# Performance work log

Measured on AMD Instinct MI355X. Metric: run time of the kernel, lower is better.

Reference implementation:

```python
import jax, jax.numpy as jnp
import numpy as np

H, W = 256, 256          # detector height/width (pixels)
DELX, DELY = 2.0, 2.0    # detector pixel pitch (mm)
EPS = 1e-8


def _rot(theta, phi, gamma):
    """R = Rz(theta) @ Ry(phi) @ Rx(gamma)."""
    ct, st = jnp.cos(theta), jnp.sin(theta)
    cp, sp = jnp.cos(phi), jnp.sin(phi)
    cg, sg = jnp.cos(gamma), jnp.sin(gamma)
    one = jnp.ones_like(ct); zero = jnp.zeros_like(ct)
    Rz = jnp.stack([jnp.stack([ct, -st, zero]), jnp.stack([st, ct, zero]), jnp.stack([zero, zero, one])])
    Ry = jnp.stack([jnp.stack([cp, zero, sp]), jnp.stack([zero, one, zero]), jnp.stack([-sp, zero, cp])])
    Rx = jnp.stack([jnp.stack([one, zero, zero]), jnp.stack([zero, cg, -sg]), jnp.stack([zero, sg, cg])])
    return Rz @ Ry @ Rx


def _make_xrays(sdr, rotations, translations):
    """Source point (3,) and detector-plane targets (H*W, 3)."""
    R = _rot(rotations[0], rotations[1], rotations[2])
    source = sdr * R[:, 0] + translations      # (3,)
    center = -sdr * R[:, 0] + translations     # detector center, opposite side
    u, v = R[:, 1], R[:, 2]                    # detector in-plane basis (unit)
    t = (jnp.arange(-(H // 2), H // 2, dtype=jnp.float32) + 1.0) * DELX  # (H,)
    s = (jnp.arange(-(W // 2), W // 2, dtype=jnp.float32) + 1.0) * DELY  # (W,)
    # cartesian_prod(t, s) @ [u; v]  ->  t_i * u + s_j * v   (t varies slowest)
    targets = t[:, None, None] * u + s[None, :, None] * v    # (H, W, 3)
    targets = targets.reshape(-1, 3) + center                # (H*W, 3)
    return source, targets


def _raytrace(volume, spacing, source, targets):
    """Siddon ray-tracing: line integral of volume along each source->target ray."""
    nx, ny, nz = volume.shape                       # planes per axis = n + 1
    dims = jnp.array([nx + 1, ny + 1, nz + 1], dtype=jnp.float32)
    sdd = targets - source + EPS                     # (R, 3) ray direction (unnormalized)

    # Entry/exit parametric range [alphamin, alphamax] per ray
    a0 = (0.0 * spacing - source) / sdd              # alpha at first planes
    a1 = ((dims - 1.0) * spacing - source) / sdd     # alpha at last planes
    amin = jnp.max(jnp.minimum(a0, a1), axis=-1, keepdims=True)  # (R, 1)
    amax = jnp.min(jnp.maximum(a0, a1), axis=-1, keepdims=True)  # (R, 1)

    # Alphas at every axis-aligned plane intersection
    ax = (jnp.arange(nx + 1, dtype=jnp.float32) * spacing[0] - source[0]) / sdd[:, 0:1]
    ay = (jnp.arange(ny + 1, dtype=jnp.float32) * spacing[1] - source[1]) / sdd[:, 1:2]
    az = (jnp.arange(nz + 1, dtype=jnp.float32) * spacing[2] - source[2]) / sdd[:, 2:3]
    alphas = jnp.concatenate([ax, ay, az], axis=-1)  # (R, P) with P = nx+ny+nz+3

    # Out-of-range alphas -> amax (amax is itself a kept plane intersection, so the
    # extra trailing segments have zero length; equivalent to the torch NaN trick
    # but NaN-free, so gradients stay clean).
    good = (alphas >= amin) & (alphas <= amax)
    alphas = jnp.where(good, alphas, amax)
    alphas = jnp.sort(alphas, axis=-1)

    amid = 0.5 * (alphas[:, :-1] + alphas[:, 1:])    # (R, P-1) segment midpoints
    step = jnp.diff(alphas, axis=-1)                 # (R, P-1) segment lengths (alpha units)

    # Voxel containing each midpoint (trunc == floor for in-volume points)
    pts = source + amid[..., None] * sdd[:, None, :] # (R, P-1, 3)
    idx = jnp.trunc(pts / spacing).astype(jnp.int32)
    idx = jnp.clip(idx, 0, jnp.array([nx - 1, ny - 1, nz - 1], dtype=jnp.int32))
    vox = volume[idx[..., 0], idx[..., 1], idx[..., 2]]  # (R, P-1)

    drr = jnp.sum(vox * step, axis=-1)               # (R,)
    raylength = jnp.linalg.norm(sdd, axis=-1)        # convert alpha units -> mm
    return drr * raylength


def setup_inputs() -> dict:
    key = jax.random.key(0)
    volume = jax.random.uniform(key, (256, 256, 256), dtype=jnp.float32)  # CT attenuation
    spacing = jnp.ones((3,), dtype=jnp.float32)
    sdr = jnp.asarray(300.0, dtype=jnp.float32)
    rotations = jnp.array([np.pi, 0.0, np.pi / 2], dtype=jnp.float32)     # theta, phi, gamma
    translations = jnp.array([128.0, 128.0, 128.0], dtype=jnp.float32)    # volume center
    return {"volume": volume, "spacing": spacing, "sdr": sdr,
            "rotations": rotations, "translations": translations}


def reference(volume, spacing, sdr, rotations, translations):
    source, targets = _make_xrays(sdr, rotations, translations)
    return _raytrace(volume, spacing, source, targets)  # (H*W,)
```

## Files before the change

kernel.cpp:

```cpp
#include <hip/hip_runtime.h>
#include <math.h>


#define NPLANE 256
constexpr int TPR = 16;

__device__ __forceinline__ float palpha(int i, float sp, float src, float rd) {
    return fmaf((float)i, sp, -src) * rd;
}

__global__ __launch_bounds__(256) void drr_kernel(
    const float* __restrict__ vol,
    const float* __restrict__ spacing,
    const float* __restrict__ sdrp,
    const float* __restrict__ rot,
    const float* __restrict__ trans,
    float* __restrict__ out)
{
    int gid  = blockIdx.x * blockDim.x + threadIdx.x;
    int part = gid & (TPR - 1);
    int rl   = gid / TPR;

    float theta = rot[0], phi = rot[1], gam = rot[2];
    float ct = cosf(theta), st = sinf(theta);
    float cp = cosf(phi),   sp_ = sinf(phi);
    float cg = cosf(gam),   sg = sinf(gam);

    float r0x = ct * cp, r0y = st * cp, r0z = -sp_;
    float ux = ct * sp_ * sg - st * cg, uy = st * sp_ * sg + ct * cg, uz = cp * sg;
    float vx = ct * sp_ * cg + st * sg, vy = st * sp_ * cg - ct * sg, vz = cp * cg;

    float cost_u = fabsf(ux) * 65536.f + fabsf(uy) * 256.f + fabsf(uz);
    float cost_v = fabsf(vx) * 65536.f + fabsf(vy) * 256.f + fabsf(vz);
    bool tfast = cost_u < cost_v;
    int ti = tfast ? (rl & 255) : (rl >> 8);
    int si = tfast ? (rl >> 8) : (rl & 255);

    float sdr = sdrp[0];
    float tx = trans[0], ty = trans[1], tz = trans[2];

    float sx = sdr * r0x + tx,  sy = sdr * r0y + ty,  sz = sdr * r0z + tz;
    float cxx = -sdr * r0x + tx, cxy = -sdr * r0y + ty, cxz = -sdr * r0z + tz;

    float tval = (float)(ti - 127) * 2.0f;
    float sval = (float)(si - 127) * 2.0f;

    float gx = tval * ux + sval * vx + cxx;
    float gy = tval * uy + sval * vy + cxy;
    float gz = tval * uz + sval * vz + cxz;

    float sdx = gx - sx + 1e-8f;
    float sdy = gy - sy + 1e-8f;
    float sdz = gz - sz + 1e-8f;

    float spx = spacing[0], spy = spacing[1], spz = spacing[2];

    float rdx = 1.0f / sdx, rdy = 1.0f / sdy, rdz = 1.0f / sdz;

    float a0x = palpha(0, spx, sx, rdx), a1x = palpha(NPLANE, spx, sx, rdx);
    float a0y = palpha(0, spy, sy, rdy), a1y = palpha(NPLANE, spy, sy, rdy);
    float a0z = palpha(0, spz, sz, rdz), a1z = palpha(NPLANE, spz, sz, rdz);

    float amin = fmaxf(fmaxf(fminf(a0x, a1x), fminf(a0y, a1y)), fminf(a0z, a1z));
    float amax = fminf(fminf(fmaxf(a0x, a1x), fmaxf(a0y, a1y)), fmaxf(a0z, a1z));

    float acc = 0.f;

    if (amax > amin) {
        float range = amax - amin;
        constexpr float inv = 1.0f / (float)TPR;
        float lo = fmaf(range, (float)part * inv, amin);
        float hi = (part == TPR - 1) ? INFINITY
                                     : fmaf(range, (float)(part + 1) * inv, amin);
        float end = fminf(hi, amax);

        int ix, iy, iz, dix, diy, diz;
        float nxx, nxy, nxz;

        #define SETUP(SP, SRC, SDD, RD, I, DI, NXT)                                \
        {                                                                          \
            float q = fmaf(lo, SDD, SRC) / (SP);                                   \
            q = fminf(fmaxf(q, -1.f), 257.f);                                      \
            if ((SDD) > 0.f) {                                                     \
                DI = 1;                                                            \
                I = (int)ceilf(q);                                                 \
                while (I > 0 && palpha(I - 1, SP, SRC, RD) >= lo) --I;             \
                while (I <= NPLANE && palpha(I, SP, SRC, RD) < lo) ++I;            \
                NXT = (I <= NPLANE) ? palpha(I, SP, SRC, RD) : INFINITY;           \
            } else {                                                               \
                DI = -1;                                                           \
                I = (int)floorf(q);                                                \
                while (I < NPLANE && palpha(I + 1, SP, SRC, RD) >= lo) ++I;        \
                while (I >= 0 && palpha(I, SP, SRC, RD) < lo) --I;                 \
                NXT = (I >= 0) ? palpha(I, SP, SRC, RD) : INFINITY;                \
            }                                                                      \
        }

        SETUP(spx, sx, sdx, rdx, ix, dix, nxx)
        SETUP(spy, sy, sdy, rdy, iy, diy, nxy)
        SETUP(spz, sz, sdz, rdz, iz, diz, nxz)
        #undef SETUP

        float ispx = 1.0f / spx, ispy = 1.0f / spy, ispz = 1.0f / spz;

        #define ADVANCE_MERGE()                                                    \
            if (nxx == cur) { ix += dix;                                           \
                nxx = ((unsigned)ix <= NPLANE) ? palpha(ix, spx, sx, rdx)          \
                                               : INFINITY; }                       \
            if (nxy == cur) { iy += diy;                                           \
                nxy = ((unsigned)iy <= NPLANE) ? palpha(iy, spy, sy, rdy)          \
                                               : INFINITY; }                       \
            if (nxz == cur) { iz += diz;                                           \
                nxz = ((unsigned)iz <= NPLANE) ? palpha(iz, spz, sz, rdz)          \
                                               : INFINITY; }

        #define SEG_ADDR(CUR, E, ADDR)                                             \
        {                                                                          \
            float amid = 0.5f * ((CUR) + (E));                                     \
            float pxv = fmaf(amid, sdx, sx) * ispx;                                \
            float pyv = fmaf(amid, sdy, sy) * ispy;                                \
            float pzv = fmaf(amid, sdz, sz) * ispz;                                \
            int jx = (int)pxv; jx = jx < 0 ? 0 : (jx > 255 ? 255 : jx);            \
            int jy = (int)pyv; jy = jy < 0 ? 0 : (jy > 255 ? 255 : jy);            \
            int jz = (int)pzv; jz = jz < 0 ? 0 : (jz > 255 ? 255 : jz);            \
            ADDR = (jx << 16) + (jy << 8) + jz;                                    \
        }

        float cur = fminf(fminf(nxx, nxy), nxz);

        if (cur < end) {
            ADVANCE_MERGE();
            float nxt = fminf(fminf(nxx, nxy), nxz);
            float e   = fminf(nxt, amax);
            int addr; SEG_ADDR(cur, e, addr)
            float pstep = e - cur;
            float pval  = vol[addr];
            cur = nxt;

            while (cur < end) {
                ADVANCE_MERGE();
                nxt = fminf(fminf(nxx, nxy), nxz);
                e   = fminf(nxt, amax);
                int addr2; SEG_ADDR(cur, e, addr2)
                float nval = vol[addr2];
                acc = fmaf(pval, pstep, acc);
                pval  = nval;
                pstep = e - cur;
                cur = nxt;
            }
            acc = fmaf(pval, pstep, acc);
        }
        #undef ADVANCE_MERGE
        #undef SEG_ADDR
    }

    for (int off = TPR / 2; off > 0; off >>= 1)
        acc += __shfl_down(acc, off, TPR);

    if (part == 0) {
        float rl2 = sqrtf(sdx * sdx + sdy * sdy + sdz * sdz);
        out[ti * 256 + si] = acc * rl2;
    }
}

extern "C" void kernel_launch(void* const* d_in, const int* in_sizes, int n_in,
                              void* d_out, int out_size, void* d_ws, size_t ws_size,
                              hipStream_t stream) {
    const float* vol     = (const float*)d_in[0];
    const float* spacing = (const float*)d_in[1];
    const float* sdr     = (const float*)d_in[2];
    const float* rot     = (const float*)d_in[3];
    const float* trans   = (const float*)d_in[4];
    float* out = (float*)d_out;

    int total = 256 * 256 * TPR;
    drr_kernel<<<total / 256, 256, 0, stream>>>(vol, spacing, sdr, rot, trans, out);
}
```

Before: 67.39 us.

## Remap ray segments across warps, swizzle blocks, unroll traversal loop, shared-memory reduction

```diff
diff --git a/kernel.cpp b/kernel.cpp
--- a/kernel.cpp
+++ b/kernel.cpp
@@ -3,13 +3,17 @@
 
 
 #define NPLANE 256
-constexpr int TPR = 16;
+constexpr int TPR   = 16;
+constexpr int BLOCK = 1024;
 
 __device__ __forceinline__ float palpha(int i, float sp, float src, float rd) {
     return fmaf((float)i, sp, -src) * rd;
 }
+__device__ __forceinline__ float palpha_f(float fi, float sp, float nsrc, float rd) {
+    return fmaf(fi, sp, nsrc) * rd;
+}
 
-__global__ __launch_bounds__(256) void drr_kernel(
+__global__ __launch_bounds__(BLOCK) void drr_kernel(
     const float* __restrict__ vol,
     const float* __restrict__ spacing,
     const float* __restrict__ sdrp,
@@ -17,9 +21,11 @@
     const float* __restrict__ trans,
     float* __restrict__ out)
 {
-    int gid  = blockIdx.x * blockDim.x + threadIdx.x;
-    int part = gid & (TPR - 1);
-    int rl   = gid / TPR;
+    int tid   = threadIdx.x;
+    int lb    = ((int)blockIdx.x * 397) & 1023;
+    int part  = (tid >> 6) & (TPR - 1);
+    int rlane = tid & 63;
+    int rl    = rlane | (lb << 6);
 
     float theta = rot[0], phi = rot[1], gam = rot[2];
     float ct = cosf(theta), st = sinf(theta);
@@ -54,7 +60,6 @@
     float sdz = gz - sz + 1e-8f;
 
     float spx = spacing[0], spy = spacing[1], spz = spacing[2];
-
     float rdx = 1.0f / sdx, rdy = 1.0f / sdy, rdz = 1.0f / sdz;
 
     float a0x = palpha(0, spx, sx, rdx), a1x = palpha(NPLANE, spx, sx, rdx);
@@ -74,7 +79,7 @@
                                      : fmaf(range, (float)(part + 1) * inv, amin);
         float end = fminf(hi, amax);
 
-        int ix, iy, iz, dix, diy, diz;
+        int iix, iiy, iiz, dix, diy, diz;
         float nxx, nxy, nxz;
 
         #define SETUP(SP, SRC, SDD, RD, I, DI, NXT)                                \
@@ -96,25 +101,23 @@
             }                                                                      \
         }
 
-        SETUP(spx, sx, sdx, rdx, ix, dix, nxx)
-        SETUP(spy, sy, sdy, rdy, iy, diy, nxy)
-        SETUP(spz, sz, sdz, rdz, iz, diz, nxz)
+        SETUP(spx, sx, sdx, rdx, iix, dix, nxx)
+        SETUP(spy, sy, sdy, rdy, iiy, diy, nxy)
+        SETUP(spz, sz, sdz, rdz, iiz, diz, nxz)
         #undef SETUP
+
+        float fix = (float)iix, fiy = (float)iiy, fiz = (float)iiz;
+        float dfx = (float)dix, dfy = (float)diy, dfz = (float)diz;
+        float nsx = -sx, nsy = -sy, nsz = -sz;
 
         float ispx = 1.0f / spx, ispy = 1.0f / spy, ispz = 1.0f / spz;
 
-        #define ADVANCE_MERGE()                                                    \
-            if (nxx == cur) { ix += dix;                                           \
-                nxx = ((unsigned)ix <= NPLANE) ? palpha(ix, spx, sx, rdx)          \
-                                               : INFINITY; }                       \
-            if (nxy == cur) { iy += diy;                                           \
-                nxy = ((unsigned)iy <= NPLANE) ? palpha(iy, spy, sy, rdy)          \
-                                               : INFINITY; }                       \
-            if (nxz == cur) { iz += diz;                                           \
-                nxz = ((unsigned)iz <= NPLANE) ? palpha(iz, spz, sz, rdz)          \
-                                               : INFINITY; }
+        #define ADV()                                                              \
+            if (nxx == cur) { fix += dfx; nxx = palpha_f(fix, spx, nsx, rdx); }    \
+            if (nxy == cur) { fiy += dfy; nxy = palpha_f(fiy, spy, nsy, rdy); }    \
+            if (nxz == cur) { fiz += dfz; nxz = palpha_f(fiz, spz, nsz, rdz); }
 
-        #define SEG_ADDR(CUR, E, ADDR)                                             \
+        #define SEG(CUR, E, ADDR)                                                  \
         {                                                                          \
             float amid = 0.5f * ((CUR) + (E));                                     \
             float pxv = fmaf(amid, sdx, sx) * ispx;                                \
@@ -129,37 +132,53 @@
         float cur = fminf(fminf(nxx, nxy), nxz);
 
         if (cur < end) {
-            ADVANCE_MERGE();
+            ADV();
             float nxt = fminf(fminf(nxx, nxy), nxz);
             float e   = fminf(nxt, amax);
-            int addr; SEG_ADDR(cur, e, addr)
-            float pstep = e - cur;
-            float pval  = vol[addr];
+            int a; SEG(cur, e, a)
+            float sA = e - cur;
+            float vA = vol[a];
             cur = nxt;
 
             while (cur < end) {
-                ADVANCE_MERGE();
+                ADV();
                 nxt = fminf(fminf(nxx, nxy), nxz);
                 e   = fminf(nxt, amax);
-                int addr2; SEG_ADDR(cur, e, addr2)
-                float nval = vol[addr2];
-                acc = fmaf(pval, pstep, acc);
-                pval  = nval;
-                pstep = e - cur;
+                SEG(cur, e, a)
+                float vB = vol[a];
+                acc = fmaf(vA, sA, acc);
+                float sB = e - cur;
+                cur = nxt;
+                if (cur >= end) { acc = fmaf(vB, sB, acc); goto traced; }
+
+                ADV();
+                nxt = fminf(fminf(nxx, nxy), nxz);
+                e   = fminf(nxt, amax);
+                SEG(cur, e, a)
+                vA = vol[a];
+                acc = fmaf(vB, sB, acc);
+                sA = e - cur;
                 cur = nxt;
             }
-            acc = fmaf(pval, pstep, acc);
+            acc = fmaf(vA, sA, acc);
+            traced: ;
         }
-        #undef ADVANCE_MERGE
-        #undef SEG_ADDR
+        #undef ADV
+        #undef SEG
     }
 
-    for (int off = TPR / 2; off > 0; off >>= 1)
-        acc += __shfl_down(acc, off, TPR);
+    __shared__ float red[BLOCK];
+    red[tid] = acc;
+    __syncthreads();
+    #pragma unroll
+    for (int off = TPR / 2; off > 0; off >>= 1) {
+        if (part < off) red[tid] = red[tid] + red[tid + off * 64];
+        __syncthreads();
+    }
 
     if (part == 0) {
         float rl2 = sqrtf(sdx * sdx + sdy * sdy + sdz * sdz);
-        out[ti * 256 + si] = acc * rl2;
+        out[ti * 256 + si] = red[tid] * rl2;
     }
 }
 
@@ -173,6 +192,6 @@
     const float* trans   = (const float*)d_in[4];
     float* out = (float*)d_out;
 
-    int total = 256 * 256 * TPR;
-    drr_kernel<<<total / 256, 256, 0, stream>>>(vol, spacing, sdr, rot, trans, out);
+    int nblocks = 256 * 256 * TPR / BLOCK;
+    drr_kernel<<<nblocks, BLOCK, 0, stream>>>(vol, spacing, sdr, rot, trans, out);
 }
```

Measured after the change: 72.64 us. +7.8%, slower.
